# Kernel optimization log

Hardware: AMD Instinct MI355X
Metric: run time of the kernel (lower is better)

The kernel has to match this reference:

```python
import jax, jax.numpy as jnp
import numpy as np

# ---- dims (match init_kwargs / mamba_ssm Mamba2 defaults) ----
VOCAB = 32000
D_MODEL = 256
N_LAYERS = 2
D_STATE = 64   # N
D_CONV = 4
EXPAND = 2
MAX_SEQ = 1024
HEADDIM = 64   # P (Mamba2 default)
D_INNER = EXPAND * D_MODEL            # 512
NHEADS = D_INNER // HEADDIM           # 8
CONV_DIM = D_INNER + 2 * D_STATE      # 640 (ngroups=1)
D_IN_PROJ = 2 * D_INNER + 2 * D_STATE + NHEADS  # 1160
B, L = 2, 1024
EPS = 1e-5


def setup_inputs() -> dict:
    key = jax.random.key(0)
    ks = jax.random.split(key, 16)
    s = 0.02
    input_ids = jax.random.randint(ks[0], (B, L), 0, VOCAB)
    attention_mask = jnp.ones((B, L), jnp.float32)
    tok_emb = jax.random.normal(ks[1], (VOCAB, D_MODEL)) * s
    tok_emb = tok_emb.at[0].set(0.0)  # padding_idx=0
    pos_emb = jax.random.normal(ks[2], (MAX_SEQ, D_MODEL)) * s
    # per-direction (2) x per-layer (N_LAYERS) stacked Mamba2 params
    shp = (2, N_LAYERS)
    in_proj_w = jax.random.normal(ks[3], shp + (D_IN_PROJ, D_MODEL)) * s
    conv_w = jax.random.normal(ks[4], shp + (CONV_DIM, D_CONV)) * 0.1
    conv_b = jnp.zeros(shp + (CONV_DIM,))
    dt = jax.random.uniform(ks[5], shp + (NHEADS,), minval=1e-3, maxval=1e-1)
    dt_bias = dt + jnp.log(-jnp.expm1(-dt))  # inverse softplus
    A_log = jnp.log(jax.random.uniform(ks[6], shp + (NHEADS,), minval=1.0, maxval=16.0))
    D_param = jnp.ones(shp + (NHEADS,))
    norm_w = jnp.ones(shp + (D_INNER,))
    out_proj_w = jax.random.normal(ks[7], shp + (D_MODEL, D_INNER)) * s
    fusion_w = jax.random.normal(ks[8], (2 * D_MODEL, 2 * D_MODEL)) * s
    fusion_b = jnp.zeros((2 * D_MODEL,))
    ln_w = jnp.ones((D_MODEL,))
    ln_b = jnp.zeros((D_MODEL,))
    return dict(input_ids=input_ids, attention_mask=attention_mask,
                tok_emb=tok_emb, pos_emb=pos_emb, in_proj_w=in_proj_w,
                conv_w=conv_w, conv_b=conv_b, dt_bias=dt_bias, A_log=A_log,
                D_param=D_param, norm_w=norm_w, out_proj_w=out_proj_w,
                fusion_w=fusion_w, fusion_b=fusion_b, ln_w=ln_w, ln_b=ln_b)


def _mamba2_layer(u, in_w, cw, cb, dtb, A_log, Dp, nw, ow):
    """One Mamba2 block forward; u: (B,L,D_MODEL)."""
    bsz, seqlen, _ = u.shape
    zxbcdt = u @ in_w.T                                   # (B,L,1160)
    z = zxbcdt[..., :D_INNER]
    xBC = zxbcdt[..., D_INNER:D_INNER + CONV_DIM]
    dt = jax.nn.softplus(zxbcdt[..., D_INNER + CONV_DIM:] + dtb)  # (B,L,H)
    # causal depthwise conv over time + SiLU
    xc = jax.lax.conv_general_dilated(
        xBC.transpose(0, 2, 1), cw[:, None, :], (1,), [(D_CONV - 1, 0)],
        feature_group_count=CONV_DIM, dimension_numbers=('NCH', 'OIH', 'NCH'))
    xBC = jax.nn.silu(xc.transpose(0, 2, 1) + cb)
    x = xBC[..., :D_INNER].reshape(bsz, seqlen, NHEADS, HEADDIM)  # (B,L,H,P)
    Bm = xBC[..., D_INNER:D_INNER + D_STATE]                      # (B,L,N)
    Cm = xBC[..., D_INNER + D_STATE:]                             # (B,L,N)
    A = -jnp.exp(A_log)                                           # (H,)

    def step(h, inp):
        x_t, B_t, C_t, dt_t = inp          # (B,H,P),(B,N),(B,N),(B,H)
        dA = jnp.exp(dt_t * A)             # (B,H)
        h = h * dA[:, :, None, None] \
            + (dt_t[:, :, None] * x_t)[..., None] * B_t[:, None, None, :]
        y_t = jnp.einsum('bhpn,bn->bhp', h, C_t)
        return h, y_t

    h0 = jnp.zeros((bsz, NHEADS, HEADDIM, D_STATE), u.dtype)
    xs = (x.transpose(1, 0, 2, 3), Bm.transpose(1, 0, 2),
          Cm.transpose(1, 0, 2), dt.transpose(1, 0, 2))
    _, ys = jax.lax.scan(step, h0, xs)                 # (L,B,H,P)
    y = ys.transpose(1, 0, 2, 3) + Dp[None, None, :, None] * x
    y = y.reshape(bsz, seqlen, D_INNER)
    # gated RMSNorm (norm_before_gate=False)
    y = y * jax.nn.silu(z)
    y = y * jax.lax.rsqrt(jnp.mean(y * y, -1, keepdims=True) + EPS) * nw
    return y @ ow.T


def _stack(h, params, d):
    (in_w, cw, cb, dtb, alog, Dp, nw, ow) = params
    for i in range(N_LAYERS):
        h = _mamba2_layer(h, in_w[d, i], cw[d, i], cb[d, i], dtb[d, i],
                          alog[d, i], Dp[d, i], nw[d, i], ow[d, i])
    return h


def reference(input_ids, attention_mask, tok_emb, pos_emb, in_proj_w, conv_w,
              conv_b, dt_bias, A_log, D_param, norm_w, out_proj_w,
              fusion_w, fusion_b, ln_w, ln_b):
    bsz, seqlen = input_ids.shape
    h = tok_emb[input_ids] + pos_emb[:seqlen][None]        # (B,L,D)
    h = h * attention_mask[..., None]                      # dropout = identity (eval)
    params = (in_proj_w, conv_w, conv_b, dt_bias, A_log, D_param, norm_w, out_proj_w)
    fwd = _stack(h, params, 0)
    bwd = jnp.flip(_stack(jnp.flip(h, 1), params, 1), 1)
    combined = jnp.concatenate([fwd, bwd], -1)             # (B,L,2D)
    gate = jax.nn.sigmoid(combined @ fusion_w.T + fusion_b)
    gf, gb = gate[..., :D_MODEL], gate[..., D_MODEL:]
    fused = gf * fwd + gb * bwd
    mu = jnp.mean(fused, -1, keepdims=True)
    var = jnp.mean((fused - mu) ** 2, -1, keepdims=True)
    return (fused - mu) * jax.lax.rsqrt(var + EPS) * ln_w + ln_b
```

## Files before the change

### kernel.cpp

```cpp
#include <hip/hip_runtime.h>
#include <cstddef>

#define LSEQ    1024
#define DMODEL  256
#define DINNER  512
#define DSTATE  64
#define NHEADS  8
#define HEADDIM 64
#define CONVDIM 640
#define DINPROJ 1160
#define ROWS    2048
#define EPSF    1e-5f
#define NC      32
#define LC      32
#define XBCW    648
#define HROW    131072

#define WIN  593920
#define WOUT 262144
#define WF   262144
#define PSI  296960
#define PSO  131072
#define LSTRIDE 1712128

typedef _Float16 f16;
typedef f16   v8h __attribute__((ext_vector_type(8)));
typedef f16   v4h __attribute__((ext_vector_type(4)));
typedef float v4f __attribute__((ext_vector_type(4)));
#define MFMA16(a, b, c) __builtin_amdgcn_mfma_f32_16x16x32_f16(a, b, c, 0, 0, 0)

__device__ __forceinline__ float sigmoidf_(float x) { return 1.0f / (1.0f + expf(-x)); }
__device__ __forceinline__ float siluf_(float x)    { return x / (1.0f + expf(-x)); }
__device__ __forceinline__ float softplusf_(float x) {
    return x > 0.0f ? x + log1pf(expf(-x)) : log1pf(expf(x));
}
__device__ __forceinline__ void split16(float v, f16& h, f16& l) {
    h = (f16)v;
    l = (f16)((v - (float)h) * 4096.0f);
}

__device__ __forceinline__ float4 conv4_(const float* __restrict__ xbcd,
                                         const float* __restrict__ cwl,
                                         const float* __restrict__ cbl,
                                         int base, int tg, int ch0) {
    float4 acc = *(const float4*)&cbl[ch0];
    float4 cw0 = *(const float4*)&cwl[(ch0 + 0) * 4];
    float4 cw1 = *(const float4*)&cwl[(ch0 + 1) * 4];
    float4 cw2 = *(const float4*)&cwl[(ch0 + 2) * 4];
    float4 cw3 = *(const float4*)&cwl[(ch0 + 3) * 4];
    const float* w0 = (const float*)&cw0;
    const float* w1 = (const float*)&cw1;
    const float* w2 = (const float*)&cw2;
    const float* w3 = (const float*)&cw3;
#pragma unroll
    for (int k = 0; k < 4; ++k) {
        int ts = tg - 3 + k;
        if (ts >= 0) {
            float4 xv = *(const float4*)&xbcd[(size_t)(base + ts) * XBCW + ch0];
            acc.x = fmaf(xv.x, w0[k], acc.x);
            acc.y = fmaf(xv.y, w1[k], acc.y);
            acc.z = fmaf(xv.z, w2[k], acc.z);
            acc.w = fmaf(xv.w, w3[k], acc.w);
        }
    }
    return acc;
}

__global__ __launch_bounds__(256) void embed_kernel(
    const int* __restrict__ ids, const float* __restrict__ mask,
    const float* __restrict__ tok, const float* __restrict__ pos,
    f16* __restrict__ uh, f16* __restrict__ ul) {
    int row = blockIdx.x;
    int d = threadIdx.x;
    int b = row >> 10, t = row & 1023;
    int id = ids[row];
    float v = tok[(size_t)id * DMODEL + d] + pos[(size_t)t * DMODEL + d];
    v *= mask[row];
    f16 h, l; split16(v, h, l);
    size_t fwd = (size_t)row * DMODEL + d;
    size_t bwd = (size_t)ROWS * DMODEL + ((size_t)(b << 10) + (1023 - t)) * DMODEL + d;
    uh[fwd] = h; ul[fwd] = l;
    uh[bwd] = h; ul[bwd] = l;
}

__global__ __launch_bounds__(256) void wconv_kernel(
    const float* __restrict__ inw, const float* __restrict__ ow, const float* __restrict__ fw,
    f16* __restrict__ wb, int total) {
    int idx = (blockIdx.x * 256 + threadIdx.x) * 4;
#pragma unroll
    for (int e = idx; e < idx + 4; ++e) {
        if (e >= total) break;
        float v; f16 *dh, *dl; int off;
        if (e < 2 * (WIN + WOUT)) {
            int layer = e / (WIN + WOUT);
            int r = e - layer * (WIN + WOUT);
            if (r < WIN) {
                int d = r / PSI, rr = r - d * PSI;
                v = inw[(size_t)(d * 2 + layer) * PSI + rr];
                dh = wb + (size_t)layer * LSTRIDE; dl = dh + WIN; off = r;
            } else {
                int r2 = r - WIN;
                int d = r2 / PSO, rr = r2 - d * PSO;
                v = ow[(size_t)(d * 2 + layer) * PSO + rr];
                dh = wb + (size_t)layer * LSTRIDE + 2 * WIN; dl = dh + WOUT; off = r2;
            }
        } else {
            int e3 = e - 2 * (WIN + WOUT);
            v = fw[e3];
            dh = wb + 2 * (size_t)LSTRIDE; dl = dh + WF; off = e3;
        }
        f16 h, l; split16(v, h, l);
        dh[off] = h; dl[off] = l;
    }
}

__global__ __launch_bounds__(256) void gemm_f16x3(
    const f16* __restrict__ Ah, const f16* __restrict__ Al, long sA,
    const f16* __restrict__ Wh, const f16* __restrict__ Wl, long sW,
    int N, int K, int Nsplit,
    float* __restrict__ O0, int ld0, long sO0,
    float* __restrict__ O1, int ld1, long sO1,
    f16* __restrict__ Ph, f16* __restrict__ Pl, int ldP, long sP,
    int has32, int haspair, int flipcomb) {
    int dir = blockIdx.z;
    Ah += (size_t)dir * sA; Al += (size_t)dir * sA;
    Wh += (size_t)dir * sW; Wl += (size_t)dir * sW;
    if (has32)  { O0 += (size_t)dir * sO0; O1 += (size_t)dir * sO1; }
    if (haspair){ Ph += (size_t)dir * sP;  Pl += (size_t)dir * sP; }

    __shared__ f16 sm[4 * 64 * 72];
    f16* As_h = sm;
    f16* As_l = sm + 64 * 72;
    f16* Ws_h = sm + 2 * 64 * 72;
    f16* Ws_l = sm + 3 * 64 * 72;

    int tid = threadIdx.x;
    int m0 = blockIdx.x * 64, n0 = blockIdx.y * 64;
    int srow = tid >> 2, sseg = tid & 3;
    int lane = tid & 63, w = tid >> 6;
    int wrow = (w >> 1) * 32, wcol = (w & 1) * 32;
    int q = lane >> 4, r16 = lane & 15;
    bool wok = (n0 + srow) < N;

    v4f accM[2][2], accX[2][2];
#pragma unroll
    for (int i = 0; i < 2; ++i)
#pragma unroll
        for (int j = 0; j < 2; ++j) { accM[i][j] = (v4f)0.0f; accX[i][j] = (v4f)0.0f; }

    for (int k0 = 0; k0 < K; k0 += 64) {
        size_t aoff = (size_t)(m0 + srow) * K + k0 + sseg * 16;
        float4 ah0 = *(const float4*)&Ah[aoff];
        float4 ah1 = *(const float4*)&Ah[aoff + 8];
        float4 al0 = *(const float4*)&Al[aoff];
        float4 al1 = *(const float4*)&Al[aoff + 8];
        float4 wh0 = make_float4(0.f,0.f,0.f,0.f), wh1 = wh0, wl0 = wh0, wl1 = wh0;
        if (wok) {
            size_t woff = (size_t)(n0 + srow) * K + k0 + sseg * 16;
            wh0 = *(const float4*)&Wh[woff];
            wh1 = *(const float4*)&Wh[woff + 8];
            wl0 = *(const float4*)&Wl[woff];
            wl1 = *(const float4*)&Wl[woff + 8];
        }
        __syncthreads();
        int d = srow * 72 + sseg * 16;
        *(float4*)&As_h[d] = ah0; *(float4*)&As_h[d + 8] = ah1;
        *(float4*)&As_l[d] = al0; *(float4*)&As_l[d + 8] = al1;
        *(float4*)&Ws_h[d] = wh0; *(float4*)&Ws_h[d + 8] = wh1;
        *(float4*)&Ws_l[d] = wl0; *(float4*)&Ws_l[d + 8] = wl1;
        __syncthreads();

#pragma unroll
        for (int ks = 0; ks < 64; ks += 32) {
            v8h fa_h[2], fa_l[2], fb_h[2], fb_l[2];
#pragma unroll
            for (int i = 0; i < 2; ++i) {
                int ra = (wrow + i * 16 + r16) * 72 + ks + q * 8;
                int rb = (wcol + i * 16 + r16) * 72 + ks + q * 8;
                fa_h[i] = *(const v8h*)&As_h[ra];
                fa_l[i] = *(const v8h*)&As_l[ra];
                fb_h[i] = *(const v8h*)&Ws_h[rb];
                fb_l[i] = *(const v8h*)&Ws_l[rb];
            }
#pragma unroll
            for (int i = 0; i < 2; ++i)
#pragma unroll
                for (int j = 0; j < 2; ++j) {
                    accM[i][j] = MFMA16(fa_h[i], fb_h[j], accM[i][j]);
                    accX[i][j] = MFMA16(fa_h[i], fb_l[j], accX[i][j]);
                    accX[i][j] = MFMA16(fa_l[i], fb_h[j], accX[i][j]);
                }
        }
    }

    const float cs = 1.0f / 4096.0f;
#pragma unroll
    for (int i = 0; i < 2; ++i)
#pragma unroll
        for (int j = 0; j < 2; ++j) {
            int nn = n0 + wcol + j * 16 + r16;
            if (nn < N) {
#pragma unroll
                for (int r = 0; r < 4; ++r) {
                    float v = accM[i][j][r] + accX[i][j][r] * cs;
                    int mm = m0 + wrow + i * 16 + q * 4 + r;
                    if (has32) {
                        if (nn < Nsplit) O0[(size_t)mm * ld0 + nn] = v;
                        else             O1[(size_t)mm * ld1 + (nn - Nsplit)] = v;
                    }
                    if (haspair) {
                        f16 h, l; split16(v, h, l);
                        if (flipcomb) {
                            int bb = mm >> 10, tt_ = mm & 1023;
                            size_t drow = dir == 0 ? (size_t)mm : (size_t)((bb << 10) + (1023 - tt_));
                            size_t dcol = dir == 0 ? (size_t)nn : (size_t)(nn + 256);
                            Ph[drow * 512 + dcol] = h;
                            Pl[drow * 512 + dcol] = l;
                        } else {
                            Ph[(size_t)mm * ldP + nn] = h;
                            Pl[(size_t)mm * ldP + nn] = l;
                        }
                    }
                }
            }
        }
}

__global__ __launch_bounds__(256) void scan_chunk_kernel(
    const float* __restrict__ xbc, const float* __restrict__ cw, const float* __restrict__ cb,
    const float* __restrict__ dtb, float* __restrict__ y,
    const float* __restrict__ Alog, const float* __restrict__ Dp,
    float* __restrict__ H, float* __restrict__ cumb, float* __restrict__ Cbuf, int layer) {
    __shared__ f16 Chs[32 * 72], Cls[32 * 72], Bhs[32 * 72], Bls[32 * 72];
    __shared__ f16 Xth[64 * 40], Xtl[64 * 40];
    __shared__ f16 Bvh[64 * 40], Bvl[64 * 40];
    __shared__ f16 Gph[32 * 40], Gpl[32 * 40];
    __shared__ float sLC[32], sRD[32], sV[32];

    int blk = blockIdx.x;
    int u = blk >> 5, c = blk & 31;
    int dir = u >> 4, b = (u >> 3) & 1, h = u & 7;
    int tid = threadIdx.x;
    int w = tid >> 6, lane = tid & 63;
    int pi = dir * 2 + layer;
    float Av = -expf(Alog[pi * NHEADS + h]);
    float Dv = Dp[pi * NHEADS + h];
    const float* xbcd = xbc + (size_t)dir * ROWS * XBCW;
    const float* cwl = cw + (size_t)pi * CONVDIM * 4;
    const float* cbl = cb + (size_t)pi * CONVDIM;
    float dtbh = dtb[pi * NHEADS + h];
    float* yd = y + (size_t)dir * ROWS * DINNER;
    int t0 = c * LC, base = b << 10;
    const float cs = 1.0f / 4096.0f;

    if (w == 0) {
        int tp = lane & 31;
        float dtraw = xbcd[(size_t)(base + t0 + tp) * XBCW + CONVDIM + h];
        float dt_l = softplusf_(dtraw + dtbh);
        float dA_l = expf(dt_l * Av);
        float cum_l = dA_l;
#pragma unroll
        for (int off = 1; off < 32; off <<= 1) {
            float o = __shfl_up(cum_l, off);
            if (tp >= off) cum_l *= o;
        }
        float lclast = __shfl(cum_l, 31);
        if (lane < 32) {
            cumb[(u << 10) + t0 + lane] = cum_l;
            float rl = 1.0f / cum_l;
            sLC[lane] = cum_l;
            sRD[lane] = rl * dt_l;
            sV[lane]  = lclast * rl * dt_l * 4096.0f;
        }
    }
    __syncthreads();

#pragma unroll
    for (int j = 0; j < 4; ++j) {
        int idx = j * 256 + tid;
        int tr = idx >> 5, c4 = idx & 31;
        int ch0 = 512 + c4 * 4;
        float4 a = conv4_(xbcd, cwl, cbl, base, t0 + tr, ch0);
        float e[4] = {siluf_(a.x), siluf_(a.y), siluf_(a.z), siluf_(a.w)};
        float vs = sV[tr];
        f16 hq[4], lq[4];
#pragma unroll
        for (int k = 0; k < 4; ++k) split16(e[k], hq[k], lq[k]);
        int col0 = c4 * 4;
        if (col0 < 64) {
            *(v4h*)&Bhs[tr * 72 + col0] = *(v4h*)hq;
            *(v4h*)&Bls[tr * 72 + col0] = *(v4h*)lq;
#pragma unroll
            for (int k = 0; k < 4; ++k) {
                f16 h2, l2; split16(e[k] * vs, h2, l2);
                Bvh[(col0 + k) * 40 + tr] = h2;
                Bvl[(col0 + k) * 40 + tr] = l2;
            }
        } else {
            *(v4h*)&Chs[tr * 72 + col0 - 64] = *(v4h*)hq;
            *(v4h*)&Cls[tr * 72 + col0 - 64] = *(v4h*)lq;
            if (h == 0)
                *(float4*)&Cbuf[((size_t)dir * ROWS + base + t0 + tr) * 64 + (col0 - 64)] =
                    make_float4(e[0], e[1], e[2], e[3]);
        }
    }
#pragma unroll
    for (int j = 0; j < 2; ++j) {
        int idx = j * 256 + tid;
        int sr = idx >> 4, c4 = idx & 15;
        int ch0 = h * HEADDIM + c4 * 4;
        float4 a = conv4_(xbcd, cwl, cbl, base, t0 + sr, ch0);
        float e[4] = {siluf_(a.x), siluf_(a.y), siluf_(a.z), siluf_(a.w)};
#pragma unroll
        for (int k = 0; k < 4; ++k) {
            f16 hh, ll; split16(e[k], hh, ll);
            Xth[(c4 * 4 + k) * 40 + sr] = hh;
            Xtl[(c4 * 4 + k) * 40 + sr] = ll;
        }
    }
    __syncthreads();

    int q = lane >> 4, r16 = lane & 15;

    {
        int ti = w >> 1, si = w & 1;
        v4f gM = (v4f)0.0f, gX = (v4f)0.0f;
#pragma unroll
        for (int ks = 0; ks < 64; ks += 32) {
            int ra = (ti * 16 + r16) * 72 + ks + q * 8;
            int rb = (si * 16 + r16) * 72 + ks + q * 8;
            v8h ca  = *(const v8h*)&Chs[ra];
            v8h cl2 = *(const v8h*)&Cls[ra];
            v8h ba  = *(const v8h*)&Bhs[rb];
            v8h bl2 = *(const v8h*)&Bls[rb];
            gM = MFMA16(ca, ba, gM);
            gX = MFMA16(ca, bl2, gX);
            gX = MFMA16(cl2, ba, gX);
        }
#pragma unroll
        for (int r = 0; r < 4; ++r) {
            int t = ti * 16 + q * 4 + r;
            int s = si * 16 + r16;
            float g = gM[r] + gX[r] * cs;
            float wgt = (s <= t) ? sLC[t] * sRD[s] * 4096.0f : 0.0f;
            f16 hh, ll; split16(g * wgt, hh, ll);
            Gph[t * 40 + s] = hh;
            Gpl[t * 40 + s] = ll;
        }
    }
    __syncthreads();

    {
        int ti = w >> 1;
        int ra = (ti * 16 + r16) * 40 + q * 8;
        v8h ga = *(const v8h*)&Gph[ra];
        v8h gl = *(const v8h*)&Gpl[ra];
#pragma unroll
        for (int jj = 0; jj < 2; ++jj) {
            int pj = (w & 1) * 2 + jj;
            int rb = (pj * 16 + r16) * 40 + q * 8;
            v8h xa = *(const v8h*)&Xth[rb];
            v8h xl = *(const v8h*)&Xtl[rb];
            v4f m = (v4f)0.0f, x2 = (v4f)0.0f;
            m  = MFMA16(ga, xa, m);
            x2 = MFMA16(ga, xl, x2);
            x2 = MFMA16(gl, xa, x2);
#pragma unroll
            for (int r = 0; r < 4; ++r) {
                int t = ti * 16 + q * 4 + r;
                int pp = pj * 16 + r16;
                float xv = (float)Xth[pp * 40 + t] + cs * (float)Xtl[pp * 40 + t];
                float val = (m[r] + x2[r] * cs) * cs + Dv * xv;
                yd[(size_t)(base + t0 + t) * DINNER + h * HEADDIM + pp] = val;
            }
        }
    }

    {
        float* Hb = H + (size_t)c * HROW + (size_t)u * 4096;
        int ni = w;
        int ra = (ni * 16 + r16) * 40 + q * 8;
        v8h ba  = *(const v8h*)&Bvh[ra];
        v8h bl2 = *(const v8h*)&Bvl[ra];
#pragma unroll
        for (int pj = 0; pj < 4; ++pj) {
            int rb = (pj * 16 + r16) * 40 + q * 8;
            v8h xa = *(const v8h*)&Xth[rb];
            v8h xl = *(const v8h*)&Xtl[rb];
            v4f m = (v4f)0.0f, x2 = (v4f)0.0f;
            m  = MFMA16(ba, xa, m);
            x2 = MFMA16(ba, xl, x2);
            x2 = MFMA16(bl2, xa, x2);
#pragma unroll
            for (int r = 0; r < 4; ++r) {
                int n = ni * 16 + q * 4 + r;
                int pp = pj * 16 + r16;
                Hb[pp * 64 + n] = (m[r] + x2[r] * cs) * cs;
            }
        }
    }
}

__global__ __launch_bounds__(256) void carry_kernel(
    float* __restrict__ H, const float* __restrict__ cumb) {
    int blk = blockIdx.x;
    int u = blk >> 4;
    int e = ((blk & 15) << 8) + threadIdx.x;
    size_t off = (size_t)u * 4096 + e;
    float carry = 0.f;
#pragma unroll 4
    for (int c = 0; c < NC; ++c) {
        float Pc = cumb[(u << 10) + c * LC + (LC - 1)];
        float* p = H + (size_t)c * HROW + off;
        float ev = *p;
        *p = carry;
        carry = fmaf(Pc, carry, ev);
    }
}

__global__ __launch_bounds__(128) void fix_kernel(
    const float* __restrict__ Cbuf, float* __restrict__ y,
    const float* __restrict__ H, const float* __restrict__ cumb) {
    __shared__ float sC[LC * 64];
    __shared__ float sCum[LC];
    int blk = blockIdx.x;
    int u = blk / (NC - 1);
    int c = blk % (NC - 1) + 1;
    int dir = u >> 4, b = (u >> 3) & 1, h = u & 7;
    int tid = threadIdx.x;
    int w = tid >> 6, p = tid & 63;
    const float* Cb = Cbuf + (size_t)dir * ROWS * 64;
    float* yd = y + (size_t)dir * ROWS * DINNER;
    int t0 = c * LC, base = b << 10;
    if (tid < LC) sCum[tid] = cumb[(u << 10) + t0 + tid];
#pragma unroll
    for (int j = 0; j < 4; ++j) {
        int f4 = j * 128 + tid;
        int trow = f4 >> 4, col4 = f4 & 15;
        float4 v = *(const float4*)&Cb[(size_t)(base + t0 + trow) * 64 + col4 * 4];
        *(float4*)&sC[trow * 64 + col4 * 4] = v;
    }
    const float* Hb = H + (size_t)c * HROW + (size_t)u * 4096 + p * 64;
    float hin[DSTATE];
#pragma unroll
    for (int n = 0; n < DSTATE; n += 4) {
        float4 v = *(const float4*)&Hb[n];
        hin[n] = v.x; hin[n + 1] = v.y; hin[n + 2] = v.z; hin[n + 3] = v.w;
    }
    __syncthreads();
#pragma unroll 2
    for (int tt = w * 16; tt < w * 16 + 16; ++tt) {
        float cumt = sCum[tt];
        const float* Cs = &sC[tt * 64];
        float y0 = 0.f, y1 = 0.f, y2 = 0.f, y3 = 0.f;
#pragma unroll
        for (int n = 0; n < DSTATE; n += 4) {
            y0 = fmaf(hin[n],     Cs[n],     y0);
            y1 = fmaf(hin[n + 1], Cs[n + 1], y1);
            y2 = fmaf(hin[n + 2], Cs[n + 2], y2);
            y3 = fmaf(hin[n + 3], Cs[n + 3], y3);
        }
        size_t yi = (size_t)(base + t0 + tt) * DINNER + h * HEADDIM + p;
        yd[yi] += cumt * ((y0 + y1) + (y2 + y3));
    }
}

__global__ __launch_bounds__(256) void gate_rms_kernel(
    const float* __restrict__ y, const float* __restrict__ zbuf,
    const float* __restrict__ nw, f16* __restrict__ yh, f16* __restrict__ yl, int layer) {
    int row = blockIdx.x;
    int dir = blockIdx.y;
    const float* zrow = zbuf + ((size_t)dir * ROWS + row) * DINNER;
    const float* yrow = y + ((size_t)dir * ROWS + row) * DINNER;
    f16* yhr = yh + ((size_t)dir * ROWS + row) * DINNER;
    f16* ylr = yl + ((size_t)dir * ROWS + row) * DINNER;
    const float* nwl = nw + (dir * 2 + layer) * DINNER;
    int tid = threadIdx.x;
    int i0 = tid, i1 = tid + 256;
    float g0 = yrow[i0] * siluf_(zrow[i0]);
    float g1 = yrow[i1] * siluf_(zrow[i1]);
    __shared__ float red[256];
    red[tid] = fmaf(g0, g0, g1 * g1);
    __syncthreads();
    for (int s = 128; s > 0; s >>= 1) {
        if (tid < s) red[tid] += red[tid + s];
        __syncthreads();
    }
    float scale = 1.0f / sqrtf(red[0] / (float)DINNER + EPSF);
    float v0 = g0 * scale * nwl[i0];
    float v1 = g1 * scale * nwl[i1];
    f16 h, l;
    split16(v0, h, l); yhr[i0] = h; ylr[i0] = l;
    split16(v1, h, l); yhr[i1] = h; ylr[i1] = l;
}

__global__ __launch_bounds__(256) void fusion_ln2_kernel(
    const float* __restrict__ u32, const float* __restrict__ gate,
    const float* __restrict__ fb, const float* __restrict__ lnw,
    const float* __restrict__ lnb, float* __restrict__ out) {
    int row = blockIdx.x;
    int b = row >> 10, t = row & 1023;
    int tid = threadIdx.x;
    float f  = u32[(size_t)row * DMODEL + tid];
    float bw = u32[(size_t)ROWS * DMODEL + ((size_t)(b << 10) + (1023 - t)) * DMODEL + tid];
    float g0 = sigmoidf_(gate[(size_t)row * 512 + tid] + fb[tid]);
    float g1 = sigmoidf_(gate[(size_t)row * 512 + 256 + tid] + fb[256 + tid]);
    float fused = g0 * f + g1 * bw;
    __shared__ float red[256];
    red[tid] = fused;
    __syncthreads();
    for (int s = 128; s > 0; s >>= 1) {
        if (tid < s) red[tid] += red[tid + s];
        __syncthreads();
    }
    float mu = red[0] / (float)DMODEL;
    __syncthreads();
    float d = fused - mu;
    red[tid] = d * d;
    __syncthreads();
    for (int s = 128; s > 0; s >>= 1) {
        if (tid < s) red[tid] += red[tid + s];
        __syncthreads();
    }
    float var = red[0] / (float)DMODEL;
    out[(size_t)row * DMODEL + tid] = d * (1.0f / sqrtf(var + EPSF)) * lnw[tid] + lnb[tid];
}

extern "C" void kernel_launch(void* const* d_in, const int* in_sizes, int n_in,
                              void* d_out, int out_size, void* d_ws, size_t ws_size,
                              hipStream_t stream) {
    const int*   ids  = (const int*)d_in[0];
    const float* mask = (const float*)d_in[1];
    const float* tok  = (const float*)d_in[2];
    const float* pos  = (const float*)d_in[3];
    const float* inw  = (const float*)d_in[4];
    const float* cw   = (const float*)d_in[5];
    const float* cb   = (const float*)d_in[6];
    const float* dtb  = (const float*)d_in[7];
    const float* alog = (const float*)d_in[8];
    const float* dpar = (const float*)d_in[9];
    const float* nw   = (const float*)d_in[10];
    const float* ow   = (const float*)d_in[11];
    const float* fw   = (const float*)d_in[12];
    const float* fb   = (const float*)d_in[13];
    const float* lnw  = (const float*)d_in[14];
    const float* lnb  = (const float*)d_in[15];

    float* ws = (float*)d_ws;
    float* zbuf = ws;
    float* xbc  = ws +  2097152;
    float* ybuf = ws +  4751360;
    f16*   yh   = (f16*)(ws +  6848512);
    f16*   yl   = (f16*)(ws +  7897088);
    float* gate = ws +  8945664;
    f16*   uh   = (f16*)(ws +  9994240);
    f16*   ul   = (f16*)(ws + 11042816);
    f16*   wb   = (f16*)(ws + 12091392);
    float* H    = ws + 14065664;
    float* cumb = ws + 18259968;
    float* Cbuf = ws + 18292736;
    float* u32  = ybuf;
    f16*   combh = (f16*)(ybuf + 1048576);
    f16*   combl = (f16*)(ybuf + 1572864);
    f16*   wfh = wb + 2 * (size_t)LSTRIDE;
    f16*   wfl = wfh + WF;

    int wtotal = 2 * (WIN + WOUT) + WF;
    wconv_kernel<<<(wtotal + 1023) / 1024, 256, 0, stream>>>(inw, ow, fw, wb, wtotal);
    embed_kernel<<<ROWS, DMODEL, 0, stream>>>(ids, mask, tok, pos, uh, ul);

    for (int layer = 0; layer < 2; ++layer) {
        f16* wih = wb + (size_t)layer * LSTRIDE;
        f16* wil = wih + WIN;
        f16* woh = wb + (size_t)layer * LSTRIDE + 2 * WIN;
        f16* wol = woh + WOUT;

        dim3 g1(ROWS / 64, (DINPROJ + 63) / 64, 2);
        gemm_f16x3<<<g1, 256, 0, stream>>>(
            uh, ul, (long)ROWS * DMODEL,
            wih, wil, (long)PSI,
            DINPROJ, DMODEL, DINNER,
            zbuf, DINNER, (long)ROWS * DINNER,
            xbc, XBCW, (long)ROWS * XBCW,
            (f16*)nullptr, (f16*)nullptr, 0, 0L,
            1, 0, 0);

        scan_chunk_kernel<<<32 * NC, 256, 0, stream>>>(
            xbc, cw, cb, dtb, ybuf, alog, dpar, H, cumb, Cbuf, layer);
        carry_kernel<<<32 * 16, 256, 0, stream>>>(H, cumb);
        fix_kernel<<<32 * (NC - 1), 128, 0, stream>>>(Cbuf, ybuf, H, cumb);
        gate_rms_kernel<<<dim3(ROWS, 2), 256, 0, stream>>>(ybuf, zbuf, nw, yh, yl, layer);

        dim3 g2(ROWS / 64, DMODEL / 64, 2);
        if (layer == 0) {
            gemm_f16x3<<<g2, 256, 0, stream>>>(
                yh, yl, (long)ROWS * DINNER,
                woh, wol, (long)PSO,
                DMODEL, DINNER, DMODEL,
                u32, DMODEL, (long)ROWS * DMODEL,
                u32, DMODEL, (long)ROWS * DMODEL,
                uh, ul, DMODEL, (long)ROWS * DMODEL,
                1, 1, 0);
        } else {
            gemm_f16x3<<<g2, 256, 0, stream>>>(
                yh, yl, (long)ROWS * DINNER,
                woh, wol, (long)PSO,
                DMODEL, DINNER, DMODEL,
                u32, DMODEL, (long)ROWS * DMODEL,
                u32, DMODEL, (long)ROWS * DMODEL,
                combh, combl, 512, 0L,
                1, 1, 1);
        }
    }

    dim3 g3(ROWS / 64, 512 / 64, 1);
    gemm_f16x3<<<g3, 256, 0, stream>>>(
        combh, combl, 0L,
        wfh, wfl, 0L,
        512, 512, 512,
        gate, 512, 0L,
        gate, 512, 0L,
        (f16*)nullptr, (f16*)nullptr, 0, 0L,
        1, 0, 0);

    fusion_ln2_kernel<<<ROWS, 256, 0, stream>>>(u32, gate, fb, lnw, lnb, (float*)d_out);
}
```

Baseline: 297.2 us.

## Merge embed and weight-convert kernels; register-prefetch next K tile in GEMM

Combines the embedding kernel and the weight split-to-fp16 kernel into one launch whose blocks branch on block index, removing one launch and letting both run concurrently. The f16x3 GEMM now loads the next K tile's A/W fragments into registers while MFMAs run on the current shared tile, overlapping global latency with compute. The prefetch raises register pressure, which may reduce occupancy.

```diff
diff --git a/kernel.cpp b/kernel.cpp
--- a/kernel.cpp
+++ b/kernel.cpp
@@ -22,6 +22,8 @@
 #define PSI  296960
 #define PSO  131072
 #define LSTRIDE 1712128
+#define WTOTAL  1974272
+#define WBLOCKS 1928
 
 typedef _Float16 f16;
 typedef f16   v8h __attribute__((ext_vector_type(8)));
@@ -66,51 +68,52 @@
     return acc;
 }
 
-__global__ __launch_bounds__(256) void embed_kernel(
+__global__ __launch_bounds__(256) void prep_kernel(
     const int* __restrict__ ids, const float* __restrict__ mask,
     const float* __restrict__ tok, const float* __restrict__ pos,
-    f16* __restrict__ uh, f16* __restrict__ ul) {
-    int row = blockIdx.x;
-    int d = threadIdx.x;
-    int b = row >> 10, t = row & 1023;
-    int id = ids[row];
-    float v = tok[(size_t)id * DMODEL + d] + pos[(size_t)t * DMODEL + d];
-    v *= mask[row];
-    f16 h, l; split16(v, h, l);
-    size_t fwd = (size_t)row * DMODEL + d;
-    size_t bwd = (size_t)ROWS * DMODEL + ((size_t)(b << 10) + (1023 - t)) * DMODEL + d;
-    uh[fwd] = h; ul[fwd] = l;
-    uh[bwd] = h; ul[bwd] = l;
-}
-
-__global__ __launch_bounds__(256) void wconv_kernel(
+    f16* __restrict__ uh, f16* __restrict__ ul,
     const float* __restrict__ inw, const float* __restrict__ ow, const float* __restrict__ fw,
-    f16* __restrict__ wb, int total) {
-    int idx = (blockIdx.x * 256 + threadIdx.x) * 4;
-#pragma unroll
-    for (int e = idx; e < idx + 4; ++e) {
-        if (e >= total) break;
-        float v; f16 *dh, *dl; int off;
-        if (e < 2 * (WIN + WOUT)) {
-            int layer = e / (WIN + WOUT);
-            int r = e - layer * (WIN + WOUT);
-            if (r < WIN) {
-                int d = r / PSI, rr = r - d * PSI;
-                v = inw[(size_t)(d * 2 + layer) * PSI + rr];
-                dh = wb + (size_t)layer * LSTRIDE; dl = dh + WIN; off = r;
+    f16* __restrict__ wb) {
+    int blk = blockIdx.x;
+    if (blk < ROWS) {
+        int row = blk;
+        int d = threadIdx.x;
+        int b = row >> 10, t = row & 1023;
+        int id = ids[row];
+        float v = tok[(size_t)id * DMODEL + d] + pos[(size_t)t * DMODEL + d];
+        v *= mask[row];
+        f16 h, l; split16(v, h, l);
+        size_t fwd = (size_t)row * DMODEL + d;
+        size_t bwd = (size_t)ROWS * DMODEL + ((size_t)(b << 10) + (1023 - t)) * DMODEL + d;
+        uh[fwd] = h; ul[fwd] = l;
+        uh[bwd] = h; ul[bwd] = l;
+    } else {
+        int idx = ((blk - ROWS) * 256 + threadIdx.x) * 4;
+#pragma unroll
+        for (int e = idx; e < idx + 4; ++e) {
+            if (e >= WTOTAL) break;
+            float v; f16 *dh, *dl; int off;
+            if (e < 2 * (WIN + WOUT)) {
+                int layer = e / (WIN + WOUT);
+                int r = e - layer * (WIN + WOUT);
+                if (r < WIN) {
+                    int d = r / PSI, rr = r - d * PSI;
+                    v = inw[(size_t)(d * 2 + layer) * PSI + rr];
+                    dh = wb + (size_t)layer * LSTRIDE; dl = dh + WIN; off = r;
+                } else {
+                    int r2 = r - WIN;
+                    int d = r2 / PSO, rr = r2 - d * PSO;
+                    v = ow[(size_t)(d * 2 + layer) * PSO + rr];
+                    dh = wb + (size_t)layer * LSTRIDE + 2 * WIN; dl = dh + WOUT; off = r2;
+                }
             } else {
-                int r2 = r - WIN;
-                int d = r2 / PSO, rr = r2 - d * PSO;
-                v = ow[(size_t)(d * 2 + layer) * PSO + rr];
-                dh = wb + (size_t)layer * LSTRIDE + 2 * WIN; dl = dh + WOUT; off = r2;
+                int e3 = e - 2 * (WIN + WOUT);
+                v = fw[e3];
+                dh = wb + 2 * (size_t)LSTRIDE; dl = dh + WF; off = e3;
             }
-        } else {
-            int e3 = e - 2 * (WIN + WOUT);
-            v = fw[e3];
-            dh = wb + 2 * (size_t)LSTRIDE; dl = dh + WF; off = e3;
-        }
-        f16 h, l; split16(v, h, l);
-        dh[off] = h; dl[off] = l;
+            f16 h, l; split16(v, h, l);
+            dh[off] = h; dl[off] = l;
+        }
     }
 }
 
@@ -148,20 +151,24 @@
 #pragma unroll
         for (int j = 0; j < 2; ++j) { accM[i][j] = (v4f)0.0f; accX[i][j] = (v4f)0.0f; }
 
-    for (int k0 = 0; k0 < K; k0 += 64) {
-        size_t aoff = (size_t)(m0 + srow) * K + k0 + sseg * 16;
-        float4 ah0 = *(const float4*)&Ah[aoff];
-        float4 ah1 = *(const float4*)&Ah[aoff + 8];
-        float4 al0 = *(const float4*)&Al[aoff];
-        float4 al1 = *(const float4*)&Al[aoff + 8];
-        float4 wh0 = make_float4(0.f,0.f,0.f,0.f), wh1 = wh0, wl0 = wh0, wl1 = wh0;
+    float4 ah0, ah1, al0, al1, wh0, wh1, wl0, wl1;
+    {
+        size_t aoff = (size_t)(m0 + srow) * K + sseg * 16;
+        ah0 = *(const float4*)&Ah[aoff];
+        ah1 = *(const float4*)&Ah[aoff + 8];
+        al0 = *(const float4*)&Al[aoff];
+        al1 = *(const float4*)&Al[aoff + 8];
+        wh0 = make_float4(0.f,0.f,0.f,0.f); wh1 = wh0; wl0 = wh0; wl1 = wh0;
         if (wok) {
-            size_t woff = (size_t)(n0 + srow) * K + k0 + sseg * 16;
+            size_t woff = (size_t)(n0 + srow) * K + sseg * 16;
             wh0 = *(const float4*)&Wh[woff];
             wh1 = *(const float4*)&Wh[woff + 8];
             wl0 = *(const float4*)&Wl[woff];
             wl1 = *(const float4*)&Wl[woff + 8];
         }
+    }
+
+    for (int k0 = 0; k0 < K; k0 += 64) {
         __syncthreads();
         int d = srow * 72 + sseg * 16;
         *(float4*)&As_h[d] = ah0; *(float4*)&As_h[d + 8] = ah1;
@@ -169,6 +176,21 @@
         *(float4*)&Ws_h[d] = wh0; *(float4*)&Ws_h[d + 8] = wh1;
         *(float4*)&Ws_l[d] = wl0; *(float4*)&Ws_l[d + 8] = wl1;
         __syncthreads();
+
+        if (k0 + 64 < K) {
+            size_t aoff = (size_t)(m0 + srow) * K + (k0 + 64) + sseg * 16;
+            ah0 = *(const float4*)&Ah[aoff];
+            ah1 = *(const float4*)&Ah[aoff + 8];
+            al0 = *(const float4*)&Al[aoff];
+            al1 = *(const float4*)&Al[aoff + 8];
+            if (wok) {
+                size_t woff = (size_t)(n0 + srow) * K + (k0 + 64) + sseg * 16;
+                wh0 = *(const float4*)&Wh[woff];
+                wh1 = *(const float4*)&Wh[woff + 8];
+                wl0 = *(const float4*)&Wl[woff];
+                wl1 = *(const float4*)&Wl[woff + 8];
+            }
+        }
 
 #pragma unroll
         for (int ks = 0; ks < 64; ks += 32) {
@@ -565,9 +587,7 @@
     f16*   wfh = wb + 2 * (size_t)LSTRIDE;
     f16*   wfl = wfh + WF;
 
-    int wtotal = 2 * (WIN + WOUT) + WF;
-    wconv_kernel<<<(wtotal + 1023) / 1024, 256, 0, stream>>>(inw, ow, fw, wb, wtotal);
-    embed_kernel<<<ROWS, DMODEL, 0, stream>>>(ids, mask, tok, pos, uh, ul);
+    prep_kernel<<<ROWS + WBLOCKS, 256, 0, stream>>>(ids, mask, tok, pos, uh, ul, inw, ow, fw, wb);
 
     for (int layer = 0; layer < 2; ++layer) {
         f16* wih = wb + (size_t)layer * LSTRIDE;
```

Result: faster. 287.4 us (-3.3%).
